# Kernel optimization log

Measured on AMD Instinct MI355X. Metric: run time of the kernel, lower is better.

Reference implementation:

```python
import jax, jax.numpy as jnp
import numpy as np

LN_EPS = 1e-5

def _layer_norm(x, gamma, beta):
    mu = jnp.mean(x, axis=-1, keepdims=True)
    var = jnp.mean(jnp.square(x - mu), axis=-1, keepdims=True)
    return (x - mu) * jax.lax.rsqrt(var + LN_EPS) * gamma + beta

def setup_inputs() -> dict:
    key = jax.random.key(0)
    ks = jax.random.split(key, 10)
    B, S, D_IN = 8, 2048, 1024
    H1, H2, C = 2048, 1024, 64
    s1 = 1.0 / np.sqrt(D_IN)
    s2 = 1.0 / np.sqrt(H1)
    s3 = 1.0 / np.sqrt(H2)
    return {
        "embeddings": jax.random.normal(ks[0], (B, S, D_IN), jnp.float32),
        "prior_evidence": jax.random.normal(ks[1], (B, C), jnp.float32),
        "W1": jax.random.uniform(ks[2], (D_IN, H1), jnp.float32, -s1, s1),
        "b1": jnp.zeros((H1,), jnp.float32),
        "g1": jnp.ones((H1,), jnp.float32),
        "beta1": jnp.zeros((H1,), jnp.float32),
        "W2": jax.random.uniform(ks[3], (H1, H2), jnp.float32, -s2, s2),
        "b2": jnp.zeros((H2,), jnp.float32),
        "g2": jnp.ones((H2,), jnp.float32),
        "beta2": jnp.zeros((H2,), jnp.float32),
        "Wh": jax.random.uniform(ks[4], (H2, C), jnp.float32, -s3, s3),
        "bh": jnp.zeros((C,), jnp.float32),
        "and_gate": jnp.ones((C,), jnp.float32),
        "or_gate": jnp.ones((C,), jnp.float32),
    }

def reference(embeddings, prior_evidence, W1, b1, g1, beta1, W2, b2, g2, beta2, Wh, bh, and_gate, or_gate):
    # feature extractor: Linear -> ReLU -> Dropout(eval: identity) -> LayerNorm, x2
    h = _layer_norm(jax.nn.relu(embeddings @ W1 + b1), g1, beta1)
    features = _layer_norm(jax.nn.relu(h @ W2 + b2), g2, beta2)  # [B,S,H2]
    d = features.shape[-1]
    scores = jnp.einsum('bsd,btd->bst', features, features) / jnp.sqrt(jnp.float32(d))
    attention_weights = jax.nn.softmax(scores, axis=-1)          # [B,S,S]
    attended = jnp.einsum('bst,btd->bsd', attention_weights, features)
    logits = attended @ Wh + bh                                   # [B,S,C]
    sig_l = jax.nn.sigmoid(logits)
    sig_p = jax.nn.sigmoid(prior_evidence)[:, None, :]            # [B,1,C] broadcasts
    and_ev = jnp.minimum(sig_l, sig_p) * and_gate
    or_ev = jnp.maximum(sig_l, sig_p) * or_gate
    logits = jnp.log((and_ev + or_ev) / 2 + 1e-10)
    return (logits, attention_weights)
```

## Files before the change

### kernel.cpp

```cpp
#include <hip/hip_runtime.h>

typedef unsigned short u16;
typedef __bf16 bf16x8 __attribute__((ext_vector_type(8)));
typedef float f32x4 __attribute__((ext_vector_type(4)));

__device__ __forceinline__ u16 f2bf(float f) {
    unsigned u = __float_as_uint(f);
    u = (u + 0x7FFFu + ((u >> 16) & 1u)) >> 16;
    return (u16)u;
}
__device__ __forceinline__ float bf2f(u16 h) {
    return __uint_as_float(((unsigned)h) << 16);
}

__device__ __forceinline__ void gld16(const u16* g, u16* l) {
    __builtin_amdgcn_global_load_lds((const __attribute__((address_space(1))) void*)g,
                                     (__attribute__((address_space(3))) void*)l, 16, 0, 0);
}

__global__ __launch_bounds__(256) void cvt_kernel(const float* __restrict__ in,
                                                  u16* __restrict__ out, long n) {
    long i = ((long)blockIdx.x * blockDim.x + threadIdx.x) * 4;
    if (i + 3 < n) {
        float4 v = *(const float4*)&in[i];
        __align__(8) u16 r[4] = {f2bf(v.x), f2bf(v.y), f2bf(v.z), f2bf(v.w)};
        *(int2*)&out[i] = *(const int2*)r;
    }
}

template <int INF32>
__global__ __launch_bounds__(256) void transpose_to_bf16(const void* __restrict__ in,
                                                         u16* __restrict__ out, int R, int C,
                                                         long inB, long outB) {
    __shared__ float tile[32][33];
    const long zi = (long)blockIdx.z * inB;
    const long zo = (long)blockIdx.z * outB;
    const int c0 = blockIdx.x * 32, r0 = blockIdx.y * 32;
    const int tx = threadIdx.x & 31;
    const int ty = threadIdx.x >> 5;
#pragma unroll
    for (int i = 0; i < 32; i += 8) {
        long idx = zi + (long)(r0 + ty + i) * C + c0 + tx;
        float v = INF32 ? ((const float*)in)[idx] : bf2f(((const u16*)in)[idx]);
        tile[ty + i][tx] = v;
    }
    __syncthreads();
#pragma unroll
    for (int i = 0; i < 32; i += 8) {
        out[zo + (long)(c0 + ty + i) * R + r0 + tx] = f2bf(tile[tx][ty + i]);
    }
}

template <int OUTBF>
__global__ __launch_bounds__(256) void gemm_nt(const u16* __restrict__ A,
                                               const u16* __restrict__ Bm,
                                               void* __restrict__ Cout, int M, int N, int K,
                                               long sA, long sB, long sC,
                                               const float* __restrict__ bias, int relu,
                                               float scale, int symm) {
    int bx, by, zz;
    if (symm) {
        const int q = gridDim.x >> 3;
        const int orig = blockIdx.x;
        const int wgid = (orig & 7) * q + (orig >> 3);
        const int NB = N >> 7;
        const int nTri = (NB * (NB + 1)) >> 1;
        zz = wgid / nTri;
        int t = wgid - zz * nTri;
        by = 0;
        int rem = NB;
        while (t >= rem) {
            t -= rem;
            --rem;
            ++by;
        }
        bx = by + t;
    } else {
        const int nx = gridDim.x;
        const int nwg = nx * gridDim.y;
        const int orig = blockIdx.y * nx + blockIdx.x;
        const int q = nwg >> 3, r = nwg & 7, xcd = orig & 7, o8 = orig >> 3;
        const int wgid = (xcd < r ? xcd * (q + 1) : r * (q + 1) + (xcd - r) * q) + o8;
        bx = wgid % nx;
        by = wgid / nx;
        zz = blockIdx.z;
    }

    __shared__ __align__(16) u16 As[128 * 64];
    __shared__ __align__(16) u16 Bs[128 * 64];
    const int tid = threadIdx.x;
    const int lane = tid & 63;
    const int wid = tid >> 6;
    const int wr = wid >> 1, wc = wid & 1;
    const int l15 = lane & 15, lg = lane >> 4;
    const long zA = (long)zz * sA;
    const long zB = (long)zz * sB;
    const long zC = (long)zz * sC;
    const int m0 = by * 128, n0 = bx * 128;

    f32x4 acc[4][4] = {};

    const int srow = tid >> 3;
    const int scol = (tid & 7) * 8;
    const u16* pa = A + zA + (long)(m0 + srow) * K + scol;
    const u16* pb = Bm + zB + (long)(n0 + srow) * K + scol;

    for (int k0 = 0; k0 < K; k0 += 64) {
#pragma unroll
        for (int i = 0; i < 4; ++i) gld16(pa + (long)i * 32 * K + k0, &As[i * 2048 + tid * 8]);
#pragma unroll
        for (int i = 0; i < 4; ++i) gld16(pb + (long)i * 32 * K + k0, &Bs[i * 2048 + tid * 8]);
        __syncthreads();
#pragma unroll
        for (int kk = 0; kk < 2; ++kk) {
            bf16x8 af[4], bfr[4];
#pragma unroll
            for (int m = 0; m < 4; ++m)
                af[m] = *(const bf16x8*)&As[(wr * 64 + m * 16 + l15) * 64 + kk * 32 + lg * 8];
#pragma unroll
            for (int n = 0; n < 4; ++n)
                bfr[n] = *(const bf16x8*)&Bs[(wc * 64 + n * 16 + l15) * 64 + kk * 32 + lg * 8];
#pragma unroll
            for (int m = 0; m < 4; ++m)
#pragma unroll
                for (int n = 0; n < 4; ++n)
                    acc[m][n] =
                        __builtin_amdgcn_mfma_f32_16x16x32_bf16(af[m], bfr[n], acc[m][n], 0, 0, 0);
        }
        __syncthreads();
    }

#pragma unroll
    for (int n = 0; n < 4; ++n) {
        const int col = n0 + wc * 64 + n * 16 + l15;
        const float bv = bias ? bias[col] : 0.0f;
#pragma unroll
        for (int m = 0; m < 4; ++m) {
            const int rowb = m0 + wr * 64 + m * 16 + lg * 4;
            float v[4];
#pragma unroll
            for (int r = 0; r < 4; ++r) {
                float f = acc[m][n][r] * scale + bv;
                if (relu) f = fmaxf(f, 0.0f);
                v[r] = f;
                if (OUTBF)
                    ((u16*)Cout)[zC + (long)(rowb + r) * N + col] = f2bf(f);
                else
                    ((float*)Cout)[zC + (long)(rowb + r) * N + col] = f;
            }
            if (!OUTBF && symm && bx > by) {
                float4 tv = make_float4(v[0], v[1], v[2], v[3]);
                *(float4*)&((float*)Cout)[zC + (long)col * N + rowb] = tv;
            }
        }
    }
}

template <int CH>
__global__ __launch_bounds__(256) void ln_wave(u16* __restrict__ x, const float* __restrict__ g,
                                               const float* __restrict__ be) {
    const int lane = threadIdx.x & 63;
    const int wid = threadIdx.x >> 6;
    const long row = (long)blockIdx.x * 4 + wid;
    u16* p = x + row * (CH * 512);
    __align__(16) u16 raw[CH][8];
    float s = 0.f, ss = 0.f;
#pragma unroll
    for (int c = 0; c < CH; ++c) {
        *(int4*)raw[c] = *(const int4*)&p[(c * 64 + lane) * 8];
#pragma unroll
        for (int j = 0; j < 8; ++j) {
            float f = bf2f(raw[c][j]);
            s += f;
            ss += f * f;
        }
    }
#pragma unroll
    for (int o = 1; o < 64; o <<= 1) {
        s += __shfl_xor(s, o);
        ss += __shfl_xor(ss, o);
    }
    const float inv = 1.0f / (float)(CH * 512);
    const float mu = s * inv;
    const float var = ss * inv - mu * mu;
    const float rs = rsqrtf(var + 1e-5f);
#pragma unroll
    for (int c = 0; c < CH; ++c) {
        const int base = (c * 64 + lane) * 8;
        float4 g0 = *(const float4*)&g[base];
        float4 g1 = *(const float4*)&g[base + 4];
        float4 b0 = *(const float4*)&be[base];
        float4 b1 = *(const float4*)&be[base + 4];
        float gv[8] = {g0.x, g0.y, g0.z, g0.w, g1.x, g1.y, g1.z, g1.w};
        float bv[8] = {b0.x, b0.y, b0.z, b0.w, b1.x, b1.y, b1.z, b1.w};
#pragma unroll
        for (int j = 0; j < 8; ++j)
            raw[c][j] = f2bf((bf2f(raw[c][j]) - mu) * rs * gv[j] + bv[j]);
        *(int4*)&p[base] = *(const int4*)raw[c];
    }
}

__global__ __launch_bounds__(256) void softmax_wave(float* __restrict__ a,
                                                    u16* __restrict__ ab) {
    const int lane = threadIdx.x & 63;
    const int wid = threadIdx.x >> 6;
    const long row = (long)blockIdx.x * 4 + wid;
    float* p = a + row * 2048;
    float v[4][8];
    float mx = -3.4e38f;
#pragma unroll
    for (int c = 0; c < 4; ++c) {
        const int base = (c * 64 + lane) * 8;
        *(float4*)&v[c][0] = *(const float4*)&p[base];
        *(float4*)&v[c][4] = *(const float4*)&p[base + 4];
#pragma unroll
        for (int j = 0; j < 8; ++j) mx = fmaxf(mx, v[c][j]);
    }
#pragma unroll
    for (int o = 1; o < 64; o <<= 1) mx = fmaxf(mx, __shfl_xor(mx, o));
    float s = 0.f;
#pragma unroll
    for (int c = 0; c < 4; ++c)
#pragma unroll
        for (int j = 0; j < 8; ++j) {
            v[c][j] = expf(v[c][j] - mx);
            s += v[c][j];
        }
#pragma unroll
    for (int o = 1; o < 64; o <<= 1) s += __shfl_xor(s, o);
    const float inv = 1.0f / s;
#pragma unroll
    for (int c = 0; c < 4; ++c) {
        const int base = (c * 64 + lane) * 8;
        __align__(16) u16 rb[8];
#pragma unroll
        for (int j = 0; j < 8; ++j) {
            v[c][j] *= inv;
            rb[j] = f2bf(v[c][j]);
        }
        *(float4*)&p[base] = *(const float4*)&v[c][0];
        *(float4*)&p[base + 4] = *(const float4*)&v[c][4];
        *(int4*)&ab[row * 2048 + base] = *(const int4*)rb;
    }
}

__global__ __launch_bounds__(256) void head_kernel(const u16* __restrict__ A,
                                                   const u16* __restrict__ WhT,
                                                   const float* __restrict__ bh,
                                                   const float* __restrict__ prior,
                                                   const float* __restrict__ ag,
                                                   const float* __restrict__ og,
                                                   float* __restrict__ out) {
    __shared__ __align__(16) u16 As[128 * 64];
    __shared__ __align__(16) u16 Bs[64 * 64];
    const int tid = threadIdx.x;
    const int lane = tid & 63;
    const int wid = tid >> 6;
    const int l15 = lane & 15, lg = lane >> 4;
    const int m0 = blockIdx.x * 128;
    const int srow = tid >> 3, scol = (tid & 7) * 8;
    const u16* pa = A + (long)(m0 + srow) * 1024 + scol;
    const u16* pb = WhT + (long)srow * 1024 + scol;

    f32x4 acc[2][4] = {};
    for (int k0 = 0; k0 < 1024; k0 += 64) {
#pragma unroll
        for (int i = 0; i < 4; ++i) gld16(pa + (long)i * 32 * 1024 + k0, &As[i * 2048 + tid * 8]);
#pragma unroll
        for (int i = 0; i < 2; ++i) gld16(pb + (long)i * 32 * 1024 + k0, &Bs[i * 2048 + tid * 8]);
        __syncthreads();
#pragma unroll
        for (int kk = 0; kk < 2; ++kk) {
            bf16x8 af[2], bfr[4];
#pragma unroll
            for (int m = 0; m < 2; ++m)
                af[m] = *(const bf16x8*)&As[(wid * 32 + m * 16 + l15) * 64 + kk * 32 + lg * 8];
#pragma unroll
            for (int n = 0; n < 4; ++n)
                bfr[n] = *(const bf16x8*)&Bs[(n * 16 + l15) * 64 + kk * 32 + lg * 8];
#pragma unroll
            for (int m = 0; m < 2; ++m)
#pragma unroll
                for (int n = 0; n < 4; ++n)
                    acc[m][n] =
                        __builtin_amdgcn_mfma_f32_16x16x32_bf16(af[m], bfr[n], acc[m][n], 0, 0, 0);
        }
        __syncthreads();
    }

#pragma unroll
    for (int n = 0; n < 4; ++n) {
        const int col = n * 16 + l15;
        const float bhv = bh[col];
        const float agv = ag[col];
        const float ogv = og[col];
#pragma unroll
        for (int m = 0; m < 2; ++m) {
#pragma unroll
            for (int r = 0; r < 4; ++r) {
                const int row = m0 + wid * 32 + m * 16 + lg * 4 + r;
                const float logit = acc[m][n][r] + bhv;
                const int b = row >> 11;
                const float sp = 1.f / (1.f + expf(-prior[b * 64 + col]));
                const float sl = 1.f / (1.f + expf(-logit));
                const float av = fminf(sl, sp) * agv;
                const float ov = fmaxf(sl, sp) * ogv;
                out[(long)row * 64 + col] = logf((av + ov) * 0.5f + 1e-10f);
            }
        }
    }
}

extern "C" void kernel_launch(void* const* d_in, const int* in_sizes, int n_in, void* d_out,
                              int out_size, void* d_ws, size_t ws_size, hipStream_t stream) {
    const float* emb = (const float*)d_in[0];
    const float* prior = (const float*)d_in[1];
    const float* W1 = (const float*)d_in[2];
    const float* b1 = (const float*)d_in[3];
    const float* g1 = (const float*)d_in[4];
    const float* be1 = (const float*)d_in[5];
    const float* W2 = (const float*)d_in[6];
    const float* b2 = (const float*)d_in[7];
    const float* g2 = (const float*)d_in[8];
    const float* be2 = (const float*)d_in[9];
    const float* Wh = (const float*)d_in[10];
    const float* bh = (const float*)d_in[11];
    const float* ag = (const float*)d_in[12];
    const float* og = (const float*)d_in[13];

    const int Bn = 8, S = 2048, DIN = 1024, H1 = 2048, H2 = 1024, Cc = 64;
    const int M = Bn * S;

    char* ws = (char*)d_ws;
    size_t off = 0;
    auto alloc = [&](size_t b) {
        size_t o = off;
        off += (b + 255) & ~(size_t)255;
        return o;
    };
    char* R0 = ws + alloc((size_t)M * H1 * 2);
    char* R1 = ws + alloc((size_t)M * DIN * 2);
    char* R2 = ws + alloc((size_t)M * H2 * 2);
    u16* W1t = (u16*)(ws + alloc((size_t)H1 * DIN * 2));
    u16* W2t = (u16*)(ws + alloc((size_t)H2 * H1 * 2));
    u16* WhT = (u16*)(ws + alloc((size_t)Cc * H2 * 2));

    u16* h = (u16*)R0;
    u16* attnb = (u16*)R0;
    u16* embb = (u16*)R1;
    u16* featT = (u16*)R1;
    u16* feat = (u16*)R2;
    u16* attd = (u16*)R2;

    float* out_logits = (float*)d_out;
    float* out_attn = out_logits + (size_t)M * Cc;

    cvt_kernel<<<(int)(((long)M * DIN) / 1024), 256, 0, stream>>>(emb, embb, (long)M * DIN);
    transpose_to_bf16<1><<<dim3(H1 / 32, DIN / 32, 1), 256, 0, stream>>>(W1, W1t, DIN, H1, 0, 0);
    transpose_to_bf16<1><<<dim3(H2 / 32, H1 / 32, 1), 256, 0, stream>>>(W2, W2t, H1, H2, 0, 0);
    transpose_to_bf16<1><<<dim3(Cc / 32, H2 / 32, 1), 256, 0, stream>>>(Wh, WhT, H2, Cc, 0, 0);
    gemm_nt<1><<<dim3(H1 / 128, M / 128, 1), 256, 0, stream>>>(embb, W1t, h, M, H1, DIN, 0, 0, 0,
                                                               b1, 1, 1.0f, 0);
    ln_wave<4><<<M / 4, 256, 0, stream>>>(h, g1, be1);
    gemm_nt<1><<<dim3(H2 / 128, M / 128, 1), 256, 0, stream>>>(h, W2t, feat, M, H2, H1, 0, 0, 0,
                                                               b2, 1, 1.0f, 0);
    ln_wave<2><<<M / 4, 256, 0, stream>>>(feat, g2, be2);
    transpose_to_bf16<0><<<dim3(H2 / 32, S / 32, Bn), 256, 0, stream>>>(
        feat, featT, S, H2, (long)S * H2, (long)H2 * S);
    {
        const int NB = S / 128;
        const int nTri = NB * (NB + 1) / 2;
        gemm_nt<0><<<dim3(nTri * Bn, 1, 1), 256, 0, stream>>>(
            feat, feat, out_attn, S, S, H2, (long)S * H2, (long)S * H2, (long)S * S, nullptr, 0,
            0.03125f, 1);
    }
    softmax_wave<<<M / 4, 256, 0, stream>>>(out_attn, attnb);
    gemm_nt<1><<<dim3(H2 / 128, S / 128, Bn), 256, 0, stream>>>(attnb, featT, attd, S, H2, S,
                                                                (long)S * S, (long)H2 * S,
                                                                (long)S * H2, nullptr, 0, 1.0f,
                                                                0);
    head_kernel<<<M / 128, 256, 0, stream>>>(attd, WhT, bh, prior, ag, og, out_logits);
}
```

Baseline: 563.7 us.

## Enlarge GEMM tiles to 256x256 with double-buffered swizzled LDS pipeline

The shared NT GEMM moves from 128x128 tiles on 256 threads to 256x256 tiles on 512 threads (8 waves, each computing 128x64). LDS is double-buffered: the next K-slice is prefetched with global_load_lds while the current one is consumed, using explicit vmcnt waits and raw s_barrier in place of two __syncthreads per iteration. LDS is laid out in 16x32 subtiles with an XOR swizzle to reduce bank conflicts, and s_setprio is raised around MFMA bursts. This aims to raise arithmetic intensity and hide load latency. The cost is 128KB of LDS per block, which limits each CU to one block, plus a heavy register load from 32 accumulators per thread. Grids shrink to 256–512 blocks, so wave-quantization effects are possible.

```diff
diff --git a/kernel.cpp b/kernel.cpp
--- a/kernel.cpp
+++ b/kernel.cpp
@@ -16,6 +16,11 @@
 __device__ __forceinline__ void gld16(const u16* g, u16* l) {
     __builtin_amdgcn_global_load_lds((const __attribute__((address_space(1))) void*)g,
                                      (__attribute__((address_space(3))) void*)l, 16, 0, 0);
+}
+
+__device__ __forceinline__ int swz(int row, int col) {
+    return ((row >> 4) * 2 + (col >> 5)) * 512 + (row & 15) * 32 +
+           ((col & 31) ^ ((row & 8) ? 16 : 0));
 }
 
 __global__ __launch_bounds__(256) void cvt_kernel(const float* __restrict__ in,
@@ -52,18 +57,18 @@
 }
 
 template <int OUTBF>
-__global__ __launch_bounds__(256) void gemm_nt(const u16* __restrict__ A,
-                                               const u16* __restrict__ Bm,
-                                               void* __restrict__ Cout, int M, int N, int K,
-                                               long sA, long sB, long sC,
-                                               const float* __restrict__ bias, int relu,
-                                               float scale, int symm) {
+__global__ __launch_bounds__(512, 2) void gemm_nt(const u16* __restrict__ A,
+                                                  const u16* __restrict__ Bm,
+                                                  void* __restrict__ Cout, int M, int N, int K,
+                                                  long sA, long sB, long sC,
+                                                  const float* __restrict__ bias, int relu,
+                                                  float scale, int symm) {
     int bx, by, zz;
     if (symm) {
         const int q = gridDim.x >> 3;
         const int orig = blockIdx.x;
         const int wgid = (orig & 7) * q + (orig >> 3);
-        const int NB = N >> 7;
+        const int NB = N >> 8;
         const int nTri = (NB * (NB + 1)) >> 1;
         zz = wgid / nTri;
         int t = wgid - zz * nTri;
@@ -86,48 +91,81 @@
         zz = blockIdx.z;
     }
 
-    __shared__ __align__(16) u16 As[128 * 64];
-    __shared__ __align__(16) u16 Bs[128 * 64];
+    __shared__ __align__(16) u16 As[2][256 * 64];
+    __shared__ __align__(16) u16 Bs[2][256 * 64];
     const int tid = threadIdx.x;
     const int lane = tid & 63;
     const int wid = tid >> 6;
-    const int wr = wid >> 1, wc = wid & 1;
+    const int wr = wid >> 2;
+    const int wc = wid & 3;
     const int l15 = lane & 15, lg = lane >> 4;
     const long zA = (long)zz * sA;
     const long zB = (long)zz * sB;
     const long zC = (long)zz * sC;
-    const int m0 = by * 128, n0 = bx * 128;
-
-    f32x4 acc[4][4] = {};
-
-    const int srow = tid >> 3;
-    const int scol = (tid & 7) * 8;
-    const u16* pa = A + zA + (long)(m0 + srow) * K + scol;
-    const u16* pb = Bm + zB + (long)(n0 + srow) * K + scol;
-
-    for (int k0 = 0; k0 < K; k0 += 64) {
-#pragma unroll
-        for (int i = 0; i < 4; ++i) gld16(pa + (long)i * 32 * K + k0, &As[i * 2048 + tid * 8]);
-#pragma unroll
-        for (int i = 0; i < 4; ++i) gld16(pb + (long)i * 32 * K + k0, &Bs[i * 2048 + tid * 8]);
-        __syncthreads();
-#pragma unroll
-        for (int kk = 0; kk < 2; ++kk) {
-            bf16x8 af[4], bfr[4];
-#pragma unroll
-            for (int m = 0; m < 4; ++m)
-                af[m] = *(const bf16x8*)&As[(wr * 64 + m * 16 + l15) * 64 + kk * 32 + lg * 8];
-#pragma unroll
-            for (int n = 0; n < 4; ++n)
-                bfr[n] = *(const bf16x8*)&Bs[(wc * 64 + n * 16 + l15) * 64 + kk * 32 + lg * 8];
-#pragma unroll
-            for (int m = 0; m < 4; ++m)
+    const int m0 = by * 256, n0 = bx * 256;
+    const u16* Ab = A + zA + (long)m0 * K;
+    const u16* Bb = Bm + zB + (long)n0 * K;
+    const int nt = K >> 6;
+
+    f32x4 acc[8][4] = {};
+
+    auto stage = [&](int t, int b) {
+#pragma unroll
+        for (int i = 0; i < 4; ++i) {
+            const int c = i * 512 + tid;
+            const int s = c >> 6, r = (c >> 2) & 15;
+            const int row = (s >> 1) * 16 + r;
+            const int col = (s & 1) * 32 + (((c & 3) * 8) ^ ((r & 8) ? 16 : 0));
+            gld16(Ab + (long)row * K + t * 64 + col, &As[b][c * 8]);
+        }
+#pragma unroll
+        for (int i = 0; i < 4; ++i) {
+            const int c = i * 512 + tid;
+            const int s = c >> 6, r = (c >> 2) & 15;
+            const int row = (s >> 1) * 16 + r;
+            const int col = (s & 1) * 32 + (((c & 3) * 8) ^ ((r & 8) ? 16 : 0));
+            gld16(Bb + (long)row * K + t * 64 + col, &Bs[b][c * 8]);
+        }
+    };
+
+    stage(0, 0);
+    for (int t = 0; t < nt; ++t) {
+        const int cur = t & 1;
+        if (t + 1 < nt) {
+            stage(t + 1, cur ^ 1);
+            asm volatile("s_waitcnt vmcnt(8)" ::: "memory");
+        } else {
+            asm volatile("s_waitcnt vmcnt(0)" ::: "memory");
+        }
+        __builtin_amdgcn_s_barrier();
+
+        bf16x8 bf[4][2];
+#pragma unroll
+        for (int n = 0; n < 4; ++n)
+#pragma unroll
+            for (int kk = 0; kk < 2; ++kk)
+                bf[n][kk] = *(const bf16x8*)&Bs[cur][swz(wc * 64 + n * 16 + l15, kk * 32 + lg * 8)];
+#pragma unroll
+        for (int mg = 0; mg < 4; ++mg) {
+            bf16x8 af[2][2];
+#pragma unroll
+            for (int mi = 0; mi < 2; ++mi)
+#pragma unroll
+                for (int kk = 0; kk < 2; ++kk)
+                    af[mi][kk] = *(const bf16x8*)&As[cur][swz(
+                        wr * 128 + mg * 32 + mi * 16 + l15, kk * 32 + lg * 8)];
+            __builtin_amdgcn_s_setprio(1);
+#pragma unroll
+            for (int mi = 0; mi < 2; ++mi)
 #pragma unroll
                 for (int n = 0; n < 4; ++n)
-                    acc[m][n] =
-                        __builtin_amdgcn_mfma_f32_16x16x32_bf16(af[m], bfr[n], acc[m][n], 0, 0, 0);
-        }
-        __syncthreads();
+#pragma unroll
+                    for (int kk = 0; kk < 2; ++kk)
+                        acc[mg * 2 + mi][n] = __builtin_amdgcn_mfma_f32_16x16x32_bf16(
+                            af[mi][kk], bf[n][kk], acc[mg * 2 + mi][n], 0, 0, 0);
+            __builtin_amdgcn_s_setprio(0);
+            __builtin_amdgcn_s_barrier();
+        }
     }
 
 #pragma unroll
@@ -135,8 +173,8 @@
         const int col = n0 + wc * 64 + n * 16 + l15;
         const float bv = bias ? bias[col] : 0.0f;
 #pragma unroll
-        for (int m = 0; m < 4; ++m) {
-            const int rowb = m0 + wr * 64 + m * 16 + lg * 4;
+        for (int m = 0; m < 8; ++m) {
+            const int rowb = m0 + wr * 128 + m * 16 + lg * 4;
             float v[4];
 #pragma unroll
             for (int r = 0; r < 4; ++r) {
@@ -149,8 +187,8 @@
                     ((float*)Cout)[zC + (long)(rowb + r) * N + col] = f;
             }
             if (!OUTBF && symm && bx > by) {
-                float4 tv = make_float4(v[0], v[1], v[2], v[3]);
-                *(float4*)&((float*)Cout)[zC + (long)col * N + rowb] = tv;
+                *(float4*)&((float*)Cout)[zC + (long)col * N + rowb] =
+                    make_float4(v[0], v[1], v[2], v[3]);
             }
         }
     }
@@ -251,8 +289,8 @@
                                                    const float* __restrict__ ag,
                                                    const float* __restrict__ og,
                                                    float* __restrict__ out) {
-    __shared__ __align__(16) u16 As[128 * 64];
-    __shared__ __align__(16) u16 Bs[64 * 64];
+    __shared__ __align__(16) u16 As2[128 * 64];
+    __shared__ __align__(16) u16 Bs2[64 * 64];
     const int tid = threadIdx.x;
     const int lane = tid & 63;
     const int wid = tid >> 6;
@@ -265,19 +303,19 @@
     f32x4 acc[2][4] = {};
     for (int k0 = 0; k0 < 1024; k0 += 64) {
 #pragma unroll
-        for (int i = 0; i < 4; ++i) gld16(pa + (long)i * 32 * 1024 + k0, &As[i * 2048 + tid * 8]);
-#pragma unroll
-        for (int i = 0; i < 2; ++i) gld16(pb + (long)i * 32 * 1024 + k0, &Bs[i * 2048 + tid * 8]);
+        for (int i = 0; i < 4; ++i) gld16(pa + (long)i * 32 * 1024 + k0, &As2[i * 2048 + tid * 8]);
+#pragma unroll
+        for (int i = 0; i < 2; ++i) gld16(pb + (long)i * 32 * 1024 + k0, &Bs2[i * 2048 + tid * 8]);
         __syncthreads();
 #pragma unroll
         for (int kk = 0; kk < 2; ++kk) {
             bf16x8 af[2], bfr[4];
 #pragma unroll
             for (int m = 0; m < 2; ++m)
-                af[m] = *(const bf16x8*)&As[(wid * 32 + m * 16 + l15) * 64 + kk * 32 + lg * 8];
+                af[m] = *(const bf16x8*)&As2[(wid * 32 + m * 16 + l15) * 64 + kk * 32 + lg * 8];
 #pragma unroll
             for (int n = 0; n < 4; ++n)
-                bfr[n] = *(const bf16x8*)&Bs[(n * 16 + l15) * 64 + kk * 32 + lg * 8];
+                bfr[n] = *(const bf16x8*)&Bs2[(n * 16 + l15) * 64 + kk * 32 + lg * 8];
 #pragma unroll
             for (int m = 0; m < 2; ++m)
 #pragma unroll
@@ -359,23 +397,23 @@
     transpose_to_bf16<1><<<dim3(H1 / 32, DIN / 32, 1), 256, 0, stream>>>(W1, W1t, DIN, H1, 0, 0);
     transpose_to_bf16<1><<<dim3(H2 / 32, H1 / 32, 1), 256, 0, stream>>>(W2, W2t, H1, H2, 0, 0);
     transpose_to_bf16<1><<<dim3(Cc / 32, H2 / 32, 1), 256, 0, stream>>>(Wh, WhT, H2, Cc, 0, 0);
-    gemm_nt<1><<<dim3(H1 / 128, M / 128, 1), 256, 0, stream>>>(embb, W1t, h, M, H1, DIN, 0, 0, 0,
+    gemm_nt<1><<<dim3(H1 / 256, M / 256, 1), 512, 0, stream>>>(embb, W1t, h, M, H1, DIN, 0, 0, 0,
                                                                b1, 1, 1.0f, 0);
     ln_wave<4><<<M / 4, 256, 0, stream>>>(h, g1, be1);
-    gemm_nt<1><<<dim3(H2 / 128, M / 128, 1), 256, 0, stream>>>(h, W2t, feat, M, H2, H1, 0, 0, 0,
+    gemm_nt<1><<<dim3(H2 / 256, M / 256, 1), 512, 0, stream>>>(h, W2t, feat, M, H2, H1, 0, 0, 0,
                                                                b2, 1, 1.0f, 0);
     ln_wave<2><<<M / 4, 256, 0, stream>>>(feat, g2, be2);
     transpose_to_bf16<0><<<dim3(H2 / 32, S / 32, Bn), 256, 0, stream>>>(
         feat, featT, S, H2, (long)S * H2, (long)H2 * S);
     {
-        const int NB = S / 128;
+        const int NB = S / 256;
         const int nTri = NB * (NB + 1) / 2;
-        gemm_nt<0><<<dim3(nTri * Bn, 1, 1), 256, 0, stream>>>(
+        gemm_nt<0><<<dim3(nTri * Bn, 1, 1), 512, 0, stream>>>(
             feat, feat, out_attn, S, S, H2, (long)S * H2, (long)S * H2, (long)S * S, nullptr, 0,
             0.03125f, 1);
     }
     softmax_wave<<<M / 4, 256, 0, stream>>>(out_attn, attnb);
-    gemm_nt<1><<<dim3(H2 / 128, S / 128, Bn), 256, 0, stream>>>(attnb, featT, attd, S, H2, S,
+    gemm_nt<1><<<dim3(H2 / 256, S / 256, Bn), 512, 0, stream>>>(attnb, featT, attd, S, H2, S,
                                                                 (long)S * S, (long)H2 * S,
                                                                 (long)S * H2, nullptr, 0, 1.0f,
                                                                 0);
```

New measurement: 513.4 us. 1.1x faster.
